# Kernel tuning notes

Measured on AMD Instinct MI355X. Metric: run time of the kernel, lower is better.

The kernel has to match this reference:

```python
import jax, jax.numpy as jnp
import numpy as np

N, E, G, H, L = 50000, 800000, 512, 128, 3
NF, EF = 128, 16
EPS = 1e-5


def _bn(x, g, b):
    # BatchNorm1d in training mode: biased batch statistics over dim 0
    mu = x.mean(0)
    var = x.var(0)
    return g * (x - mu) * jax.lax.rsqrt(var + EPS) + b


def setup_inputs() -> dict:
    key = jax.random.key(0)
    ks = jax.random.split(key, 16)
    s = 0.05
    return {
        "x": jax.random.normal(ks[0], (N, NF), jnp.float32),
        "edge_attr": jax.random.normal(ks[1], (E, EF), jnp.float32),
        "atom_W": jax.random.normal(ks[2], (NF, H), jnp.float32) * s,
        "atom_b": jnp.zeros((H,), jnp.float32),
        "vn_emb": jax.random.normal(ks[3], (H,), jnp.float32) * s,
        "conv_We": jax.random.normal(ks[4], (L, EF, H), jnp.float32) * s,
        "conv_be": jnp.zeros((L, H), jnp.float32),
        "conv_W": jax.random.normal(ks[5], (L, H, H), jnp.float32) * s,
        "conv_b": jnp.zeros((L, H), jnp.float32),
        "conv_g": jnp.ones((L, H), jnp.float32),
        "conv_beta": jnp.zeros((L, H), jnp.float32),
        "vn1_W": jax.random.normal(ks[6], (L, 2 * H, 2 * H), jnp.float32) * s,
        "vn1_b": jnp.zeros((L, 2 * H), jnp.float32),
        "vn1_g": jnp.ones((L, 2 * H), jnp.float32),
        "vn1_beta": jnp.zeros((L, 2 * H), jnp.float32),
        "vn2_W": jax.random.normal(ks[7], (L, 2 * H, H), jnp.float32) * s,
        "vn2_b": jnp.zeros((L, H), jnp.float32),
        "vn2_g": jnp.ones((L, H), jnp.float32),
        "vn2_beta": jnp.zeros((L, H), jnp.float32),
        "pred_W1": jax.random.normal(ks[8], (L * H, L * H), jnp.float32) * s,
        "pred_b1": jnp.zeros((L * H,), jnp.float32),
        "pred_W2": jax.random.normal(ks[9], (L * H, 1), jnp.float32) * s,
        "pred_b2": jnp.zeros((1,), jnp.float32),
        "edge_index": jax.random.randint(ks[10], (2, E), 0, N),
        "batch": jnp.sort(jax.random.randint(ks[11], (N,), 0, G)),
    }


def reference(x, edge_attr, atom_W, atom_b, vn_emb, conv_We, conv_be, conv_W,
              conv_b, conv_g, conv_beta, vn1_W, vn1_b, vn1_g, vn1_beta,
              vn2_W, vn2_b, vn2_g, vn2_beta, pred_W1, pred_b1, pred_W2,
              pred_b2, edge_index, batch):
    src, dst = edge_index[0], edge_index[1]
    h = x @ atom_W + atom_b                      # atom_encoder: [N, H]
    vn = jnp.broadcast_to(vn_emb, (G, H))        # virtual node per graph
    vxs = []
    for i in range(L):
        h = h + vn[batch]                         # gather virtual node by graph id
        # CombConv: edge-conditioned GIN-style message passing
        e = edge_attr @ conv_We[i] + conv_be[i]   # [E, H]
        msg = jax.nn.relu(h[src] + e)             # gather + fuse
        agg = jax.ops.segment_sum(msg, dst, num_segments=N)
        h = jax.nn.relu(_bn((h + agg) @ conv_W[i] + conv_b[i], conv_g[i], conv_beta[i]))
        # virtual node update: gather -> MLP1 -> segment pool -> MLP2
        t = jnp.concatenate([vn[batch], h], axis=-1)          # [N, 2H]
        t = jax.nn.relu(_bn(t @ vn1_W[i] + vn1_b[i], vn1_g[i], vn1_beta[i]))
        pooled = jax.ops.segment_sum(t, batch, num_segments=G)  # global_add_pool
        vn = jax.nn.relu(_bn(pooled @ vn2_W[i] + vn2_b[i], vn2_g[i], vn2_beta[i]))
        vxs.append(vn)
    hg = jnp.concatenate(vxs, axis=-1)            # JK='C': [G, L*H]
    hg = jax.nn.relu(hg @ pred_W1 + pred_b1)
    return hg @ pred_W2 + pred_b2                 # [G, 1]
```

## Files before the change

kernel.cpp:

```cpp
#include <hip/hip_runtime.h>
#include <hip/hip_fp16.h>

constexpr int N = 50000;
constexpr int E = 800000;
constexpr int G = 512;
constexpr int H = 128;
constexpr long long NH = (long long)N * H;
constexpr float EPS = 1e-5f;
constexpr int NB_SCAN = 196;

typedef _Float16 f16x8 __attribute__((ext_vector_type(8)));
typedef _Float16 f16x2 __attribute__((ext_vector_type(2)));
typedef float f32x4 __attribute__((ext_vector_type(4)));

__global__ void k_init_vn(const float* __restrict__ vn_emb, float* __restrict__ vn) {
  int idx = blockIdx.x * 256 + threadIdx.x;
  vn[idx] = vn_emb[idx & 127];
}

__global__ void k_tof16(const float* __restrict__ in, __half* __restrict__ out, int n4) {
  int i = blockIdx.x * 256 + threadIdx.x;
  if (i >= n4) return;
  float4 v = reinterpret_cast<const float4*>(in)[i];
  __half2* o = reinterpret_cast<__half2*>(out);
  o[i * 2]     = __floats2half2_rn(v.x, v.y);
  o[i * 2 + 1] = __floats2half2_rn(v.z, v.w);
}

__global__ void k_wt(const float* __restrict__ W, __half* __restrict__ Wt,
                     int ldw, int row0, int cols, long long wstride, int wtstride) {
  const float* Wl = W + (long long)blockIdx.y * wstride;
  __half* Wtl = Wt + (long long)blockIdx.y * wtstride;
  int idx = blockIdx.x * 256 + threadIdx.x;
  int k = idx & 127, c = idx >> 7;
  Wtl[c * 128 + k] = __float2half(Wl[(long long)(row0 + k) * ldw + c]);
}

__global__ void k_addvn16(__half* __restrict__ h16, const float* __restrict__ vn,
                          const int* __restrict__ batch) {
  int i2 = blockIdx.x * 256 + threadIdx.x;
  int r = i2 >> 6;
  int b = batch[r];
  __half2 hv = reinterpret_cast<__half2*>(h16)[i2];
  float2 vv = reinterpret_cast<const float2*>(vn)[(b << 6) + (i2 & 63)];
  reinterpret_cast<__half2*>(h16)[i2] =
      __floats2half2_rn(__low2float(hv) + vv.x, __high2float(hv) + vv.y);
}

__global__ void k_gstart(const int* __restrict__ batch, int* __restrict__ gstart) {
  int g = threadIdx.x;
  int lo = 0, hi = N;
  while (lo < hi) { int mid = (lo + hi) >> 1; if (batch[mid] < g) lo = mid + 1; else hi = mid; }
  gstart[g] = lo;
  if (g == 0) gstart[G] = N;
}

__global__ void k_hist(const int* __restrict__ dst, int* __restrict__ cnt) {
  int e = blockIdx.x * 256 + threadIdx.x;
  atomicAdd(&cnt[dst[e]], 1);
}

__global__ void k_scan_block(const int* __restrict__ cnt, int* __restrict__ off,
                             int* __restrict__ bsum) {
  __shared__ int s[256];
  int idx = blockIdx.x * 256 + threadIdx.x;
  int v = (idx < N) ? cnt[idx] : 0;
  s[threadIdx.x] = v;
  __syncthreads();
  for (int o = 1; o < 256; o <<= 1) {
    int t = (threadIdx.x >= o) ? s[threadIdx.x - o] : 0;
    __syncthreads();
    s[threadIdx.x] += t;
    __syncthreads();
  }
  if (idx < N) off[idx + 1] = s[threadIdx.x];
  if (threadIdx.x == 255) bsum[blockIdx.x] = s[255];
  if (idx == 0) off[0] = 0;
}

__global__ void k_scan_bsum(int* __restrict__ bsum) {
  __shared__ int s[256];
  int v = (threadIdx.x < NB_SCAN) ? bsum[threadIdx.x] : 0;
  s[threadIdx.x] = v;
  __syncthreads();
  for (int o = 1; o < 256; o <<= 1) {
    int t = (threadIdx.x >= o) ? s[threadIdx.x - o] : 0;
    __syncthreads();
    s[threadIdx.x] += t;
    __syncthreads();
  }
  if (threadIdx.x < NB_SCAN) bsum[threadIdx.x] = s[threadIdx.x];
}

__global__ void k_scan_add(int* __restrict__ off, const int* __restrict__ bsum) {
  int idx = blockIdx.x * 256 + threadIdx.x;
  if (idx < N && blockIdx.x > 0) off[idx + 1] += bsum[blockIdx.x - 1];
}

__global__ void k_scatter(const int* __restrict__ src, const int* __restrict__ dst,
                          const int* __restrict__ off, int* __restrict__ cur,
                          int* __restrict__ srcp, __half* __restrict__ eap,
                          const float* __restrict__ edge_attr) {
  int e = blockIdx.x * 256 + threadIdx.x;
  int d = dst[e];
  int p = off[d] + atomicAdd(&cur[d], 1);
  srcp[p] = src[e] * 64;
  const float4* ea4 = reinterpret_cast<const float4*>(edge_attr) + e * 4;
  float4 a0 = ea4[0], a1 = ea4[1], a2 = ea4[2], a3 = ea4[3];
  __half2* o = reinterpret_cast<__half2*>(eap + (long long)p * 16);
  o[0] = __floats2half2_rn(a0.x, a0.y);
  o[1] = __floats2half2_rn(a0.z, a0.w);
  o[2] = __floats2half2_rn(a1.x, a1.y);
  o[3] = __floats2half2_rn(a1.z, a1.w);
  o[4] = __floats2half2_rn(a2.x, a2.y);
  o[5] = __floats2half2_rn(a2.z, a2.w);
  o[6] = __floats2half2_rn(a3.x, a3.y);
  o[7] = __floats2half2_rn(a3.z, a3.w);
}

__global__ __launch_bounds__(256) void k_agg(
    const __half* __restrict__ eap, const float* __restrict__ We,
    const float* __restrict__ be, const int* __restrict__ off,
    const int* __restrict__ srcp, const __half* __restrict__ h16,
    __half* __restrict__ hpa16, int d0) {
  int tid = threadIdx.x;
  int lane = tid & 63;
  int c0 = lane * 2;
  f16x2 wc0[8], wc1[8];
#pragma unroll
  for (int kk = 0; kk < 8; ++kk) {
    f16x2 w0, w1;
    w0[0] = (_Float16)We[(2 * kk) * 128 + c0];
    w0[1] = (_Float16)We[(2 * kk + 1) * 128 + c0];
    w1[0] = (_Float16)We[(2 * kk) * 128 + c0 + 1];
    w1[1] = (_Float16)We[(2 * kk + 1) * 128 + c0 + 1];
    wc0[kk] = w0; wc1[kk] = w1;
  }
  float2 bev = reinterpret_cast<const float2*>(be)[lane];
  int d = d0 + blockIdx.x * 4 + (tid >> 6);
  int j0 = off[d], j1 = off[d + 1];
  const __half2* h2 = reinterpret_cast<const __half2*>(h16);
  const int4* e4 = reinterpret_cast<const int4*>(eap);
  float a0 = 0.f, a1 = 0.f, b0 = 0.f, b1 = 0.f;
  float p0 = 0.f, p1 = 0.f, q0 = 0.f, q1 = 0.f;
  int j = j0;
#define EDGE(J, A0, A1) do {                                                   \
    int s_ = srcp[(J)];                                                        \
    __half2 hv_ = h2[s_ + lane];                                               \
    int4 lo_ = e4[2 * (J)], hi_ = e4[2 * (J) + 1];                             \
    float ev0_ = bev.x, ev1_ = bev.y;                                          \
    ev0_ = __builtin_amdgcn_fdot2(__builtin_bit_cast(f16x2, lo_.x), wc0[0], ev0_, false); \
    ev1_ = __builtin_amdgcn_fdot2(__builtin_bit_cast(f16x2, lo_.x), wc1[0], ev1_, false); \
    ev0_ = __builtin_amdgcn_fdot2(__builtin_bit_cast(f16x2, lo_.y), wc0[1], ev0_, false); \
    ev1_ = __builtin_amdgcn_fdot2(__builtin_bit_cast(f16x2, lo_.y), wc1[1], ev1_, false); \
    ev0_ = __builtin_amdgcn_fdot2(__builtin_bit_cast(f16x2, lo_.z), wc0[2], ev0_, false); \
    ev1_ = __builtin_amdgcn_fdot2(__builtin_bit_cast(f16x2, lo_.z), wc1[2], ev1_, false); \
    ev0_ = __builtin_amdgcn_fdot2(__builtin_bit_cast(f16x2, lo_.w), wc0[3], ev0_, false); \
    ev1_ = __builtin_amdgcn_fdot2(__builtin_bit_cast(f16x2, lo_.w), wc1[3], ev1_, false); \
    ev0_ = __builtin_amdgcn_fdot2(__builtin_bit_cast(f16x2, hi_.x), wc0[4], ev0_, false); \
    ev1_ = __builtin_amdgcn_fdot2(__builtin_bit_cast(f16x2, hi_.x), wc1[4], ev1_, false); \
    ev0_ = __builtin_amdgcn_fdot2(__builtin_bit_cast(f16x2, hi_.y), wc0[5], ev0_, false); \
    ev1_ = __builtin_amdgcn_fdot2(__builtin_bit_cast(f16x2, hi_.y), wc1[5], ev1_, false); \
    ev0_ = __builtin_amdgcn_fdot2(__builtin_bit_cast(f16x2, hi_.z), wc0[6], ev0_, false); \
    ev1_ = __builtin_amdgcn_fdot2(__builtin_bit_cast(f16x2, hi_.z), wc1[6], ev1_, false); \
    ev0_ = __builtin_amdgcn_fdot2(__builtin_bit_cast(f16x2, hi_.w), wc0[7], ev0_, false); \
    ev1_ = __builtin_amdgcn_fdot2(__builtin_bit_cast(f16x2, hi_.w), wc1[7], ev1_, false); \
    A0 += fmaxf(__low2float(hv_) + ev0_, 0.f);                                 \
    A1 += fmaxf(__high2float(hv_) + ev1_, 0.f);                                \
  } while (0)
  for (; j + 3 < j1; j += 4) {
    EDGE(j, a0, a1);
    EDGE(j + 1, b0, b1);
    EDGE(j + 2, p0, p1);
    EDGE(j + 3, q0, q1);
  }
  for (; j < j1; ++j) EDGE(j, a0, a1);
#undef EDGE
  a0 += b0 + p0 + q0; a1 += b1 + p1 + q1;
  int di = d * 64 + lane;
  __half2 hd = h2[di];
  reinterpret_cast<__half2*>(hpa16)[di] =
      __floats2half2_rn(__low2float(hd) + a0, __high2float(hd) + a1);
}

template<bool HAS_BIAS, bool HAS_ROWBIAS, bool OUT_F16, bool STATS>
__global__ __launch_bounds__(256) void k_mgemm(
    const __half* __restrict__ A, const __half* __restrict__ Bt,
    const float* __restrict__ bias, const float* __restrict__ bias2,
    const float* __restrict__ rowbias, const int* __restrict__ batch,
    float* __restrict__ Cf, __half* __restrict__ Ch,
    float* __restrict__ stats, int ldc, int M) {
  __shared__ _Float16 Bsh[128][136];
  int tid = threadIdx.x;
  int m0 = blockIdx.x * 64;
  int c0 = blockIdx.y * 128;
  int wid = tid >> 6, lane = tid & 63;
  int wr = wid >> 1, wc = wid & 1;
  int lrow = lane & 15;
  int lk = (lane >> 4) * 8;

  f16x8 af[4][2];
#pragma unroll
  for (int kk = 0; kk < 4; ++kk)
#pragma unroll
    for (int fm = 0; fm < 2; ++fm)
      af[kk][fm] = *reinterpret_cast<const f16x8*>(
          A + (m0 + wr * 32 + fm * 16 + lrow) * 128 + kk * 32 + lk);

#pragma unroll
  for (int it = 0; it < 8; ++it) {
    int idx = it * 256 + tid;
    int r = idx >> 4, ck = idx & 15;
    f16x8 v = *reinterpret_cast<const f16x8*>(Bt + ((c0 + r) << 7) + ck * 8);
    *reinterpret_cast<f16x8*>(&Bsh[r][ck * 8]) = v;
  }
  __syncthreads();

  f32x4 acc[2][4];
#pragma unroll
  for (int fm = 0; fm < 2; ++fm)
#pragma unroll
    for (int fn = 0; fn < 4; ++fn) acc[fm][fn] = (f32x4){0.f, 0.f, 0.f, 0.f};

#pragma unroll
  for (int kk = 0; kk < 4; ++kk) {
    f16x8 bf[4];
#pragma unroll
    for (int fn = 0; fn < 4; ++fn)
      bf[fn] = *reinterpret_cast<const f16x8*>(&Bsh[wc * 64 + fn * 16 + lrow][kk * 32 + lk]);
#pragma unroll
    for (int fm = 0; fm < 2; ++fm)
#pragma unroll
      for (int fn = 0; fn < 4; ++fn)
        acc[fm][fn] = __builtin_amdgcn_mfma_f32_16x16x32_f16(af[kk][fm], bf[fn], acc[fm][fn], 0, 0, 0);
  }

  float ss[4], ss2[4];
#pragma unroll
  for (int fn = 0; fn < 4; ++fn) { ss[fn] = 0.f; ss2[fn] = 0.f; }
#pragma unroll
  for (int fn = 0; fn < 4; ++fn) {
    int col = c0 + wc * 64 + fn * 16 + lrow;
    float bb = HAS_BIAS ? bias[col] : 0.f;
    if (HAS_BIAS && bias2 != nullptr) bb += bias2[col];
#pragma unroll
    for (int fm = 0; fm < 2; ++fm) {
      int grb = m0 + wr * 32 + fm * 16 + (lane >> 4) * 4;
#pragma unroll
      for (int j = 0; j < 4; ++j) {
        int gr = grb + j;
        if (gr < M) {
          float v = acc[fm][fn][j] + bb;
          if (HAS_ROWBIAS)
            v += rowbias[batch[gr] * ldc + col];
          if (STATS) { ss[fn] += v; ss2[fn] += v * v; }
          if (OUT_F16)
            Ch[(long long)gr * ldc + col] = __float2half(v);
          else
            Cf[(long long)gr * ldc + col] = v;
        }
      }
    }
  }
  if (STATS) {
    __shared__ float sred[2][4][4][16];
#pragma unroll
    for (int fn = 0; fn < 4; ++fn) {
      float s = ss[fn], s2 = ss2[fn];
      s += __shfl_xor(s, 16);  s += __shfl_xor(s, 32);
      s2 += __shfl_xor(s2, 16); s2 += __shfl_xor(s2, 32);
      if (lane < 16) { sred[0][wid][fn][lane] = s; sred[1][wid][fn][lane] = s2; }
    }
    __syncthreads();
    if (wr == 0 && lane < 16) {
#pragma unroll
      for (int fn = 0; fn < 4; ++fn) {
        int col = c0 + wc * 64 + fn * 16 + lane;
        atomicAdd(&stats[col],       sred[0][wid][fn][lane] + sred[0][wid + 2][fn][lane]);
        atomicAdd(&stats[ldc + col], sred[1][wid][fn][lane] + sred[1][wid + 2][fn][lane]);
      }
    }
  }
}

template<int K, bool HAS_BIAS, bool HAS_ROWBIAS, bool RELU, bool STATS>
__global__ __launch_bounds__(256) void k_gemm(
    const float* __restrict__ A1,
    const float* __restrict__ W, int ldw,
    const float* __restrict__ bias,
    const float* __restrict__ rowbias, const int* __restrict__ batch,
    float* __restrict__ C, float* __restrict__ stats, int M) {
  __shared__ float As[32 * K];
  constexpr int K4 = K / 4;
  int tid = threadIdx.x;
  int m0 = blockIdx.x * 32;
#pragma unroll
  for (int it = 0; it < K / 32; ++it) {
    int e4 = it * 256 + tid;
    int r = e4 / K4;
    int k4 = e4 % K4;
    int gr = m0 + r;
    float4 v = make_float4(0.f, 0.f, 0.f, 0.f);
    if (gr < M) v = reinterpret_cast<const float4*>(A1)[(long long)gr * K4 + k4];
    reinterpret_cast<float4*>(As)[e4] = v;
  }
  __shared__ float cs[128], cs2[128];
  if (STATS && tid < 128) { cs[tid] = 0.f; cs2[tid] = 0.f; }
  __syncthreads();

  int cg = tid & 31;
  int rg = tid >> 5;
  int col = blockIdx.y * 128 + cg * 4;
  float4 acc[4];
#pragma unroll
  for (int j = 0; j < 4; ++j) acc[j] = make_float4(0.f, 0.f, 0.f, 0.f);
  const float4* W4 = reinterpret_cast<const float4*>(W);
  const float4* As4 = reinterpret_cast<const float4*>(As);
#pragma unroll 8
  for (int k = 0; k < K; k += 4) {
    float4 w0 = W4[((k + 0) * ldw + col) >> 2];
    float4 w1 = W4[((k + 1) * ldw + col) >> 2];
    float4 w2 = W4[((k + 2) * ldw + col) >> 2];
    float4 w3 = W4[((k + 3) * ldw + col) >> 2];
#pragma unroll
    for (int j = 0; j < 4; ++j) {
      float4 a = As4[(rg + j * 8) * K4 + (k >> 2)];
      acc[j].x += a.x * w0.x + a.y * w1.x + a.z * w2.x + a.w * w3.x;
      acc[j].y += a.x * w0.y + a.y * w1.y + a.z * w2.y + a.w * w3.y;
      acc[j].z += a.x * w0.z + a.y * w1.z + a.z * w2.z + a.w * w3.z;
      acc[j].w += a.x * w0.w + a.y * w1.w + a.z * w2.w + a.w * w3.w;
    }
  }
  float4 bb = make_float4(0.f, 0.f, 0.f, 0.f);
  if (HAS_BIAS) bb = reinterpret_cast<const float4*>(bias)[blockIdx.y * 32 + cg];
  float ps[4] = {0.f, 0.f, 0.f, 0.f}, ps2[4] = {0.f, 0.f, 0.f, 0.f};
#pragma unroll
  for (int j = 0; j < 4; ++j) {
    int gr = m0 + rg + j * 8;
    if (gr < M) {
      float4 v = acc[j];
      v.x += bb.x; v.y += bb.y; v.z += bb.z; v.w += bb.w;
      if (HAS_ROWBIAS) {
        int b = batch[gr];
        float4 rb = reinterpret_cast<const float4*>(rowbias)[((long long)b * ldw + col) >> 2];
        v.x += rb.x; v.y += rb.y; v.z += rb.z; v.w += rb.w;
      }
      if (RELU) {
        v.x = fmaxf(v.x, 0.f); v.y = fmaxf(v.y, 0.f);
        v.z = fmaxf(v.z, 0.f); v.w = fmaxf(v.w, 0.f);
      }
      if (STATS) {
        ps[0] += v.x; ps2[0] += v.x * v.x;
        ps[1] += v.y; ps2[1] += v.y * v.y;
        ps[2] += v.z; ps2[2] += v.z * v.z;
        ps[3] += v.w; ps2[3] += v.w * v.w;
      }
      reinterpret_cast<float4*>(C)[((long long)gr * ldw + col) >> 2] = v;
    }
  }
  if (STATS) {
#pragma unroll
    for (int jc = 0; jc < 4; ++jc) {
      atomicAdd(&cs[cg * 4 + jc], ps[jc]);
      atomicAdd(&cs2[cg * 4 + jc], ps2[jc]);
    }
    __syncthreads();
    if (tid < 128) {
      atomicAdd(&stats[blockIdx.y * 128 + tid], cs[tid]);
      atomicAdd(&stats[ldw + blockIdx.y * 128 + tid], cs2[tid]);
    }
  }
}

__global__ void k_bn16(const __half* __restrict__ X16, const float* __restrict__ stats,
                       const float* __restrict__ gam, const float* __restrict__ beta,
                       __half* __restrict__ out16, float invM) {
  int i2 = blockIdx.x * 256 + threadIdx.x;
  int c = (i2 & 63) * 2;
  __half2 xv = reinterpret_cast<const __half2*>(X16)[i2];
  float m0 = stats[c] * invM;
  float v0 = stats[128 + c] * invM - m0 * m0;
  float m1 = stats[c + 1] * invM;
  float v1 = stats[128 + c + 1] * invM - m1 * m1;
  float r0 = fmaxf((__low2float(xv) - m0) * rsqrtf(v0 + EPS) * gam[c] + beta[c], 0.f);
  float r1 = fmaxf((__high2float(xv) - m1) * rsqrtf(v1 + EPS) * gam[c + 1] + beta[c + 1], 0.f);
  reinterpret_cast<__half2*>(out16)[i2] = __floats2half2_rn(r0, r1);
}

__global__ void k_pool(const __half* __restrict__ z2_16, const float* __restrict__ stats,
                       const float* __restrict__ gam, const float* __restrict__ beta,
                       const int* __restrict__ gstart, float* __restrict__ pooled) {
  int g = blockIdx.x;
  int c = blockIdx.y * 128 + threadIdx.x;
  const float invM = 1.f / (float)N;
  float mean = stats[c] * invM;
  float var = stats[256 + c] * invM - mean * mean;
  float scale = rsqrtf(var + EPS) * gam[c];
  float shift = beta[c] - mean * scale;
  int r0 = gstart[g], r1 = gstart[g + 1];
  float acc = 0.f;
  for (int r = r0; r < r1; ++r) {
    float v = __half2float(z2_16[(long long)r * 256 + c]);
    acc += fmaxf(v * scale + shift, 0.f);
  }
  pooled[g * 256 + c] = acc;
}

__global__ void k_vnapply(const float* __restrict__ zvn, const float* __restrict__ stats,
                          const float* __restrict__ gam, const float* __restrict__ beta,
                          float* __restrict__ vn, float* __restrict__ hgbuf, int layer) {
  int idx = blockIdx.x * 256 + threadIdx.x;
  int c = idx & 127;
  int g = idx >> 7;
  const float invM = 1.f / (float)G;
  float mean = stats[c] * invM;
  float var = stats[128 + c] * invM - mean * mean;
  float v = fmaxf((zvn[idx] - mean) * rsqrtf(var + EPS) * gam[c] + beta[c], 0.f);
  vn[idx] = v;
  hgbuf[g * 384 + layer * 128 + c] = v;
}

__global__ void k_pred2(const float* __restrict__ hg2, const float* __restrict__ W2,
                        const float* __restrict__ b2, float* __restrict__ out) {
  int g = blockIdx.x;
  int lane = threadIdx.x;
  float s = 0.f;
  for (int k = lane; k < 384; k += 64) s += hg2[g * 384 + k] * W2[k];
  for (int off = 32; off; off >>= 1) s += __shfl_down(s, off);
  if (lane == 0) out[g] = s + b2[0];
}

extern "C" void kernel_launch(void* const* d_in, const int* in_sizes, int n_in,
                              void* d_out, int out_size, void* d_ws, size_t ws_size,
                              hipStream_t stream) {
  const float* x         = (const float*)d_in[0];
  const float* edge_attr = (const float*)d_in[1];
  const float* atom_W    = (const float*)d_in[2];
  const float* atom_b    = (const float*)d_in[3];
  const float* vn_emb    = (const float*)d_in[4];
  const float* conv_We   = (const float*)d_in[5];
  const float* conv_be   = (const float*)d_in[6];
  const float* conv_W    = (const float*)d_in[7];
  const float* conv_b    = (const float*)d_in[8];
  const float* conv_g    = (const float*)d_in[9];
  const float* conv_beta = (const float*)d_in[10];
  const float* vn1_W     = (const float*)d_in[11];
  const float* vn1_b     = (const float*)d_in[12];
  const float* vn1_g     = (const float*)d_in[13];
  const float* vn1_beta  = (const float*)d_in[14];
  const float* vn2_W     = (const float*)d_in[15];
  const float* vn2_b     = (const float*)d_in[16];
  const float* vn2_g     = (const float*)d_in[17];
  const float* vn2_beta  = (const float*)d_in[18];
  const float* pred_W1   = (const float*)d_in[19];
  const float* pred_b1   = (const float*)d_in[20];
  const float* pred_W2   = (const float*)d_in[21];
  const float* pred_b2   = (const float*)d_in[22];
  const int*   eidx      = (const int*)d_in[23];
  const int*   batch     = (const int*)d_in[24];
  const int* src = eidx;
  const int* dst = eidx + E;

  float* ws    = (float*)d_ws;
  __half* h16  = (__half*)ws;
  float* bufB  = ws + NH / 2;
  __half* hpa16= (__half*)bufB;
  __half* z16  = (__half*)(bufB + NH / 2);
  __half* x16  = z16;
  __half* z2_16= (__half*)(bufB + NH);
  float* smallz= bufB + 2 * NH;
  float* U     = smallz;
  float* pooled= U + G * 256;
  float* zvn   = pooled + G * 256;
  float* vn    = zvn + G * 128;
  float* hgbuf = vn + G * 128;
  float* hg2   = hgbuf + G * 384;
  float* statsz= hg2 + G * 384;
  int*   gstart= (int*)(statsz + 3 * 1024);
  __half* atomWt = (__half*)(gstart + 516);
  __half* convWt = atomWt + 16384;
  __half* z2Wt   = convWt + 3 * 16384;
  int*  off    = (int*)(z2Wt + 3 * 32768);
  int*  srcp   = off + 50002;
  __half* eap  = (__half*)(srcp + E);
  int* cnt  = (int*)bufB;
  int* cur  = cnt + N;
  int* bsum = cur + N;

  dim3 b256(256);

  hipMemsetAsync(cnt, 0, (size_t)(2 * N + NB_SCAN) * 4, stream);
  hipMemsetAsync(statsz, 0, 3 * 1024 * 4, stream);
  k_hist<<<E / 256, b256, 0, stream>>>(dst, cnt);
  k_scan_block<<<NB_SCAN, b256, 0, stream>>>(cnt, off, bsum);
  k_scan_bsum<<<1, b256, 0, stream>>>(bsum);
  k_scan_add<<<NB_SCAN, b256, 0, stream>>>(off, bsum);
  k_scatter<<<E / 256, b256, 0, stream>>>(src, dst, off, cur, srcp, eap, edge_attr);
  k_gstart<<<1, G, 0, stream>>>(batch, gstart);

  k_init_vn<<<G * 128 / 256, b256, 0, stream>>>(vn_emb, vn);

  k_tof16<<<(N * 128 / 4 + 255) / 256, b256, 0, stream>>>(x, x16, N * 128 / 4);
  k_wt<<<dim3(64, 1), b256, 0, stream>>>(atom_W, atomWt, 128, 0, 128, 0, 0);
  k_wt<<<dim3(64, 3), b256, 0, stream>>>(conv_W, convWt, 128, 0, 128, 16384, 16384);
  k_wt<<<dim3(128, 3), b256, 0, stream>>>(vn1_W, z2Wt, 256, 128, 256, 65536, 32768);

  k_mgemm<true, false, true, false><<<dim3(782, 1), b256, 0, stream>>>(
      x16, atomWt, atom_b, vn_emb, nullptr, nullptr, nullptr, h16, nullptr, 128, N);

  for (int i = 0; i < 3; ++i) {
    float* SZ = statsz + i * 1024;
    if (i > 0) k_addvn16<<<12500, b256, 0, stream>>>(h16, vn, batch);
    k_agg<<<6250, b256, 0, stream>>>(eap, conv_We + i * 2048, conv_be + i * 128,
                                     off, srcp, h16, hpa16, 0);
    k_agg<<<6250, b256, 0, stream>>>(eap, conv_We + i * 2048, conv_be + i * 128,
                                     off, srcp, h16, hpa16, 25000);
    k_mgemm<true, false, true, true><<<dim3(782, 1), b256, 0, stream>>>(
        hpa16, convWt + i * 16384, conv_b + i * 128, nullptr, nullptr, nullptr,
        nullptr, z16, SZ, 128, N);
    k_bn16<<<12500, b256, 0, stream>>>(z16, SZ, conv_g + i * 128, conv_beta + i * 128,
                                       h16, 1.f / (float)N);
    k_gemm<128, true, false, false, false><<<dim3(16, 2), b256, 0, stream>>>(
        vn, vn1_W + i * 256 * 256, 256, vn1_b + i * 256, nullptr, nullptr, U, nullptr, G);
    k_mgemm<false, true, true, true><<<dim3(782, 2), b256, 0, stream>>>(
        h16, z2Wt + i * 32768, nullptr, nullptr, U, batch, nullptr, z2_16,
        SZ + 256, 256, N);
    k_pool<<<dim3(G, 2), dim3(128), 0, stream>>>(
        z2_16, SZ + 256, vn1_g + i * 256, vn1_beta + i * 256, gstart, pooled);
    k_gemm<256, true, false, false, true><<<dim3(16, 1), b256, 0, stream>>>(
        pooled, vn2_W + i * 256 * 128, 128, vn2_b + i * 128, nullptr, nullptr,
        zvn, SZ + 768, G);
    k_vnapply<<<G * 128 / 256, b256, 0, stream>>>(
        zvn, SZ + 768, vn2_g + i * 128, vn2_beta + i * 128, vn, hgbuf, i);
  }
  k_gemm<384, true, false, true, false><<<dim3(16, 3), b256, 0, stream>>>(
      hgbuf, pred_W1, 384, pred_b1, nullptr, nullptr, hg2, nullptr, G);
  k_pred2<<<G, 64, 0, stream>>>(hg2, pred_W2, pred_b2, (float*)d_out);
}
```

Baseline: 1.287 ms.

## Double-buffer edge loads in aggregation, split CSR scatter, widen pool reduction

```diff
diff --git a/kernel.cpp b/kernel.cpp
--- a/kernel.cpp
+++ b/kernel.cpp
@@ -97,17 +97,23 @@
   if (idx < N && blockIdx.x > 0) off[idx + 1] += bsum[blockIdx.x - 1];
 }
 
-__global__ void k_scatter(const int* __restrict__ src, const int* __restrict__ dst,
-                          const int* __restrict__ off, int* __restrict__ cur,
-                          int* __restrict__ srcp, __half* __restrict__ eap,
-                          const float* __restrict__ edge_attr) {
+__global__ void k_scatter_idx(const int* __restrict__ dst, const int* __restrict__ off,
+                              int* __restrict__ cur, int* __restrict__ eidp) {
   int e = blockIdx.x * 256 + threadIdx.x;
   int d = dst[e];
   int p = off[d] + atomicAdd(&cur[d], 1);
-  srcp[p] = src[e] * 64;
+  eidp[p] = e;
+}
+
+__global__ void k_permute(const int* __restrict__ eidp, const int* __restrict__ src,
+                          const float* __restrict__ edge_attr,
+                          int* __restrict__ srcp, __half* __restrict__ eap) {
+  int i = blockIdx.x * 256 + threadIdx.x;
+  int e = eidp[i];
+  srcp[i] = src[e] * 64;
   const float4* ea4 = reinterpret_cast<const float4*>(edge_attr) + e * 4;
   float4 a0 = ea4[0], a1 = ea4[1], a2 = ea4[2], a3 = ea4[3];
-  __half2* o = reinterpret_cast<__half2*>(eap + (long long)p * 16);
+  __half2* o = reinterpret_cast<__half2*>(eap + (long long)i * 16);
   o[0] = __floats2half2_rn(a0.x, a0.y);
   o[1] = __floats2half2_rn(a0.z, a0.w);
   o[2] = __floats2half2_rn(a1.x, a1.y);
@@ -143,39 +149,65 @@
   const int4* e4 = reinterpret_cast<const int4*>(eap);
   float a0 = 0.f, a1 = 0.f, b0 = 0.f, b1 = 0.f;
   float p0 = 0.f, p1 = 0.f, q0 = 0.f, q1 = 0.f;
+
+#define FD(U, W, ACC) ACC = __builtin_amdgcn_fdot2(__builtin_bit_cast(f16x2, U), W, ACC, false)
+#define COMP1(LOk, HIk, HVk, A0, A1) do {                                      \
+    float ev0_ = bev.x, ev1_ = bev.y;                                          \
+    FD(LOk.x, wc0[0], ev0_); FD(LOk.x, wc1[0], ev1_);                          \
+    FD(LOk.y, wc0[1], ev0_); FD(LOk.y, wc1[1], ev1_);                          \
+    FD(LOk.z, wc0[2], ev0_); FD(LOk.z, wc1[2], ev1_);                          \
+    FD(LOk.w, wc0[3], ev0_); FD(LOk.w, wc1[3], ev1_);                          \
+    FD(HIk.x, wc0[4], ev0_); FD(HIk.x, wc1[4], ev1_);                          \
+    FD(HIk.y, wc0[5], ev0_); FD(HIk.y, wc1[5], ev1_);                          \
+    FD(HIk.z, wc0[6], ev0_); FD(HIk.z, wc1[6], ev1_);                          \
+    FD(HIk.w, wc0[7], ev0_); FD(HIk.w, wc1[7], ev1_);                          \
+    A0 += fmaxf(__low2float(HVk) + ev0_, 0.f);                                 \
+    A1 += fmaxf(__high2float(HVk) + ev1_, 0.f);                                \
+  } while (0)
+#define LOADG(S, LO, HI, HV, BASE) do {                                        \
+    _Pragma("unroll")                                                          \
+    for (int k_ = 0; k_ < 4; ++k_) {                                           \
+      S[k_] = srcp[(BASE) + k_];                                               \
+      LO[k_] = e4[2 * ((BASE) + k_)];                                          \
+      HI[k_] = e4[2 * ((BASE) + k_) + 1];                                      \
+    }                                                                          \
+    _Pragma("unroll")                                                          \
+    for (int k_ = 0; k_ < 4; ++k_) HV[k_] = h2[S[k_] + lane];                  \
+  } while (0)
+#define COMPG(LO, HI, HV) do {                                                 \
+    COMP1(LO[0], HI[0], HV[0], a0, a1);                                        \
+    COMP1(LO[1], HI[1], HV[1], b0, b1);                                        \
+    COMP1(LO[2], HI[2], HV[2], p0, p1);                                        \
+    COMP1(LO[3], HI[3], HV[3], q0, q1);                                        \
+  } while (0)
+
   int j = j0;
-#define EDGE(J, A0, A1) do {                                                   \
-    int s_ = srcp[(J)];                                                        \
-    __half2 hv_ = h2[s_ + lane];                                               \
-    int4 lo_ = e4[2 * (J)], hi_ = e4[2 * (J) + 1];                             \
-    float ev0_ = bev.x, ev1_ = bev.y;                                          \
-    ev0_ = __builtin_amdgcn_fdot2(__builtin_bit_cast(f16x2, lo_.x), wc0[0], ev0_, false); \
-    ev1_ = __builtin_amdgcn_fdot2(__builtin_bit_cast(f16x2, lo_.x), wc1[0], ev1_, false); \
-    ev0_ = __builtin_amdgcn_fdot2(__builtin_bit_cast(f16x2, lo_.y), wc0[1], ev0_, false); \
-    ev1_ = __builtin_amdgcn_fdot2(__builtin_bit_cast(f16x2, lo_.y), wc1[1], ev1_, false); \
-    ev0_ = __builtin_amdgcn_fdot2(__builtin_bit_cast(f16x2, lo_.z), wc0[2], ev0_, false); \
-    ev1_ = __builtin_amdgcn_fdot2(__builtin_bit_cast(f16x2, lo_.z), wc1[2], ev1_, false); \
-    ev0_ = __builtin_amdgcn_fdot2(__builtin_bit_cast(f16x2, lo_.w), wc0[3], ev0_, false); \
-    ev1_ = __builtin_amdgcn_fdot2(__builtin_bit_cast(f16x2, lo_.w), wc1[3], ev1_, false); \
-    ev0_ = __builtin_amdgcn_fdot2(__builtin_bit_cast(f16x2, hi_.x), wc0[4], ev0_, false); \
-    ev1_ = __builtin_amdgcn_fdot2(__builtin_bit_cast(f16x2, hi_.x), wc1[4], ev1_, false); \
-    ev0_ = __builtin_amdgcn_fdot2(__builtin_bit_cast(f16x2, hi_.y), wc0[5], ev0_, false); \
-    ev1_ = __builtin_amdgcn_fdot2(__builtin_bit_cast(f16x2, hi_.y), wc1[5], ev1_, false); \
-    ev0_ = __builtin_amdgcn_fdot2(__builtin_bit_cast(f16x2, hi_.z), wc0[6], ev0_, false); \
-    ev1_ = __builtin_amdgcn_fdot2(__builtin_bit_cast(f16x2, hi_.z), wc1[6], ev1_, false); \
-    ev0_ = __builtin_amdgcn_fdot2(__builtin_bit_cast(f16x2, hi_.w), wc0[7], ev0_, false); \
-    ev1_ = __builtin_amdgcn_fdot2(__builtin_bit_cast(f16x2, hi_.w), wc1[7], ev1_, false); \
-    A0 += fmaxf(__low2float(hv_) + ev0_, 0.f);                                 \
-    A1 += fmaxf(__high2float(hv_) + ev1_, 0.f);                                \
-  } while (0)
-  for (; j + 3 < j1; j += 4) {
-    EDGE(j, a0, a1);
-    EDGE(j + 1, b0, b1);
-    EDGE(j + 2, p0, p1);
-    EDGE(j + 3, q0, q1);
-  }
-  for (; j < j1; ++j) EDGE(j, a0, a1);
-#undef EDGE
+  if (j + 3 < j1) {
+    int sA[4], sB[4];
+    int4 loA[4], hiA[4], loB[4], hiB[4];
+    __half2 hvA[4], hvB[4];
+    LOADG(sA, loA, hiA, hvA, j);
+    j += 4;
+    bool curA = true;
+    while (j + 3 < j1) {
+      if (curA) { LOADG(sB, loB, hiB, hvB, j); COMPG(loA, hiA, hvA); }
+      else      { LOADG(sA, loA, hiA, hvA, j); COMPG(loB, hiB, hvB); }
+      curA = !curA;
+      j += 4;
+    }
+    if (curA) COMPG(loA, hiA, hvA);
+    else      COMPG(loB, hiB, hvB);
+  }
+  for (; j < j1; ++j) {
+    int s_ = srcp[j];
+    int4 lo_ = e4[2 * j], hi_ = e4[2 * j + 1];
+    __half2 hv_ = h2[s_ + lane];
+    COMP1(lo_, hi_, hv_, a0, a1);
+  }
+#undef LOADG
+#undef COMPG
+#undef COMP1
+#undef FD
   a0 += b0 + p0 + q0; a1 += b1 + p1 + q1;
   int di = d * 64 + lane;
   __half2 hd = h2[di];
@@ -390,8 +422,11 @@
 __global__ void k_pool(const __half* __restrict__ z2_16, const float* __restrict__ stats,
                        const float* __restrict__ gam, const float* __restrict__ beta,
                        const int* __restrict__ gstart, float* __restrict__ pooled) {
+  int tid = threadIdx.x;
+  int rsub = tid >> 7;
+  int cl = tid & 127;
   int g = blockIdx.x;
-  int c = blockIdx.y * 128 + threadIdx.x;
+  int c = blockIdx.y * 128 + cl;
   const float invM = 1.f / (float)N;
   float mean = stats[c] * invM;
   float var = stats[256 + c] * invM - mean * mean;
@@ -399,11 +434,15 @@
   float shift = beta[c] - mean * scale;
   int r0 = gstart[g], r1 = gstart[g + 1];
   float acc = 0.f;
-  for (int r = r0; r < r1; ++r) {
+  for (int r = r0 + rsub; r < r1; r += 4) {
     float v = __half2float(z2_16[(long long)r * 256 + c]);
     acc += fmaxf(v * scale + shift, 0.f);
   }
-  pooled[g * 256 + c] = acc;
+  __shared__ float sred[512];
+  sred[tid] = acc;
+  __syncthreads();
+  if (rsub == 0)
+    pooled[g * 256 + c] = sred[cl] + sred[128 + cl] + sred[256 + cl] + sred[384 + cl];
 }
 
 __global__ void k_vnapply(const float* __restrict__ zvn, const float* __restrict__ stats,
@@ -486,6 +525,7 @@
   int* cnt  = (int*)bufB;
   int* cur  = cnt + N;
   int* bsum = cur + N;
+  int* eidp = cur + N + 256;
 
   dim3 b256(256);
 
@@ -495,7 +535,8 @@
   k_scan_block<<<NB_SCAN, b256, 0, stream>>>(cnt, off, bsum);
   k_scan_bsum<<<1, b256, 0, stream>>>(bsum);
   k_scan_add<<<NB_SCAN, b256, 0, stream>>>(off, bsum);
-  k_scatter<<<E / 256, b256, 0, stream>>>(src, dst, off, cur, srcp, eap, edge_attr);
+  k_scatter_idx<<<E / 256, b256, 0, stream>>>(dst, off, cur, eidp);
+  k_permute<<<E / 256, b256, 0, stream>>>(eidp, src, edge_attr, srcp, eap);
   k_gstart<<<1, G, 0, stream>>>(batch, gstart);
 
   k_init_vn<<<G * 128 / 256, b256, 0, stream>>>(vn_emb, vn);
@@ -525,7 +566,7 @@
     k_mgemm<false, true, true, true><<<dim3(782, 2), b256, 0, stream>>>(
         h16, z2Wt + i * 32768, nullptr, nullptr, U, batch, nullptr, z2_16,
         SZ + 256, 256, N);
-    k_pool<<<dim3(G, 2), dim3(128), 0, stream>>>(
+    k_pool<<<dim3(G, 2), dim3(512), 0, stream>>>(
         z2_16, SZ + 256, vn1_g + i * 256, vn1_beta + i * 256, gstart, pooled);
     k_gemm<256, true, false, false, true><<<dim3(16, 1), b256, 0, stream>>>(
         pooled, vn2_W + i * 256 * 128, 128, vn2_b + i * 128, nullptr, nullptr,
```

Result: slower. 1.389 ms (+7.9%).
